# Kernel tuning notes

Measured on AMD Instinct MI355X. Metric: run time of the kernel, lower is better.

## Reference

```python
import jax, jax.numpy as jnp
import numpy as np

TEMPERATURE = 8.0  # sqrt(d_head=64)


def setup_inputs() -> dict:
    key = jax.random.key(0)
    kq, kk, kv, km = jax.random.split(key, 4)
    B, N, L, D = 2, 16, 2048, 64
    q = jax.random.normal(kq, (B, N, L, D), dtype=jnp.float32)
    k = jax.random.normal(kk, (B, N, L, D), dtype=jnp.float32)
    v = jax.random.normal(kv, (B, N, L, D), dtype=jnp.float32)
    mask = jax.random.randint(km, (B, N, L, L), 0, 2).astype(jnp.bool_)
    return {"q": q, "k": k, "v": v, "mask": mask}


def reference(q, k, v, mask):
    # attn = (q @ k^T) / temperature, shape [b, n, lq, lk]
    attn = jnp.einsum("bnqd,bnkd->bnqk", q, k) / TEMPERATURE
    attn = jnp.where(mask, -jnp.inf, attn)
    attn = jax.nn.softmax(attn, axis=-1)
    attn = jnp.where(mask, 0.0, attn)
    # dropout is identity in eval/reference mode
    output = jnp.einsum("bnqk,bnkd->bnqd", attn, v)
    return (output, attn)
```

## Files before the change

kernel.cpp:

```cpp
#include <hip/hip_runtime.h>
#include <math.h>

#define L 2048
#define D 64
#define MT 32
#define KT 128
#define NT 256
#define QSTRIDE 72
#define KSTRIDE 72
#define VSTRIDE 136
#define PSTRIDE 136

typedef short bf16x8 __attribute__((ext_vector_type(8)));
typedef float f32x4  __attribute__((ext_vector_type(4)));

__device__ inline short f2bf(float f) {
    union { float f; unsigned u; } x; x.f = f;
    unsigned r = x.u + 0x7fffu + ((x.u >> 16) & 1u);
    return (short)(r >> 16);
}

__global__ __launch_bounds__(NT) void sdpa_mfma(
    const float* __restrict__ q,
    const float* __restrict__ k,
    const float* __restrict__ v,
    const int*   __restrict__ mask,
    float* __restrict__ out,
    float* __restrict__ attn)
{
    const int bid  = blockIdx.x;
    const int bn   = bid >> 6;
    const int qt   = bid & 63;
    const int row0 = qt * MT;
    const int tid  = threadIdx.x;
    const int wave = tid >> 6;
    const int lane = tid & 63;
    const int lq   = lane & 15;
    const int lg   = lane >> 4;

    __shared__ short Qs[MT * QSTRIDE];
    __shared__ short KV[KT * KSTRIDE];
    __shared__ short Ps[MT * PSTRIDE];
    __shared__ float sums_w[4][MT];
    __shared__ float inv_s[MT];

    const float* qg = q + ((size_t)bn * L + row0) * D;
    const float* kg = k + (size_t)bn * L * D;
    const float* vg = v + (size_t)bn * L * D;
    const int*   mg = mask + ((size_t)bn * L + row0) * L;
    float*       ag = attn + ((size_t)bn * L + row0) * L;

    {
        const int r = tid >> 3, c8 = (tid & 7) * 8;
        const float4* src = (const float4*)(qg + r * D + c8);
        float4 a = src[0], b = src[1];
        bf16x8 t;
        t[0]=f2bf(a.x); t[1]=f2bf(a.y); t[2]=f2bf(a.z); t[3]=f2bf(a.w);
        t[4]=f2bf(b.x); t[5]=f2bf(b.y); t[6]=f2bf(b.z); t[7]=f2bf(b.w);
        *(bf16x8*)&Qs[r * QSTRIDE + c8] = t;
    }
    __syncthreads();

    bf16x8 qa[2][2];
    #pragma unroll
    for (int r = 0; r < 2; ++r)
        #pragma unroll
        for (int s = 0; s < 2; ++s)
            qa[r][s] = *(bf16x8*)&Qs[(r*16 + lq) * QSTRIDE + s*32 + lg*8];

    float sumreg[2][4] = {};
    for (int kt = 0; kt < L / KT; ++kt) {
        const int kb = kt * KT;
        __syncthreads();
        {
            const int r = tid >> 3, c8 = (tid & 7) * 8;
            #pragma unroll
            for (int it = 0; it < 4; ++it) {
                const int rr = r + it * 32;
                const float4* src = (const float4*)(kg + (size_t)(kb + rr) * D + c8);
                float4 a = src[0], b = src[1];
                bf16x8 t;
                t[0]=f2bf(a.x); t[1]=f2bf(a.y); t[2]=f2bf(a.z); t[3]=f2bf(a.w);
                t[4]=f2bf(b.x); t[5]=f2bf(b.y); t[6]=f2bf(b.z); t[7]=f2bf(b.w);
                *(bf16x8*)&KV[rr * KSTRIDE + c8] = t;
            }
        }
        __syncthreads();
        f32x4 acc[2][2] = {};
        #pragma unroll
        for (int s = 0; s < 2; ++s) {
            bf16x8 b0 = *(bf16x8*)&KV[((wave*2+0)*16 + lq) * KSTRIDE + s*32 + lg*8];
            bf16x8 b1 = *(bf16x8*)&KV[((wave*2+1)*16 + lq) * KSTRIDE + s*32 + lg*8];
            acc[0][0] = __builtin_amdgcn_mfma_f32_16x16x32_bf16(qa[0][s], b0, acc[0][0], 0, 0, 0);
            acc[0][1] = __builtin_amdgcn_mfma_f32_16x16x32_bf16(qa[0][s], b1, acc[0][1], 0, 0, 0);
            acc[1][0] = __builtin_amdgcn_mfma_f32_16x16x32_bf16(qa[1][s], b0, acc[1][0], 0, 0, 0);
            acc[1][1] = __builtin_amdgcn_mfma_f32_16x16x32_bf16(qa[1][s], b1, acc[1][1], 0, 0, 0);
        }
        #pragma unroll
        for (int r = 0; r < 2; ++r)
            #pragma unroll
            for (int cc = 0; cc < 2; ++cc) {
                const int col = kb + (wave*2+cc)*16 + lq;
                #pragma unroll
                for (int i = 0; i < 4; ++i) {
                    const int rowl = r*16 + lg*4 + i;
                    const int m = mg[(size_t)rowl * L + col];
                    const float e = m ? 0.f : __expf(acc[r][cc][i] * 0.125f);
                    sumreg[r][i] += e;
                }
            }
    }
    #pragma unroll
    for (int off = 1; off < 16; off <<= 1)
        #pragma unroll
        for (int r = 0; r < 2; ++r)
            #pragma unroll
            for (int i = 0; i < 4; ++i)
                sumreg[r][i] += __shfl_xor(sumreg[r][i], off, 64);
    if (lq == 0)
        #pragma unroll
        for (int r = 0; r < 2; ++r)
            #pragma unroll
            for (int i = 0; i < 4; ++i)
                sums_w[wave][r*16 + lg*4 + i] = sumreg[r][i];
    __syncthreads();
    if (tid < MT) {
        const float s = sums_w[0][tid] + sums_w[1][tid] + sums_w[2][tid] + sums_w[3][tid];
        inv_s[tid] = 1.0f / s;
    }
    __syncthreads();

    f32x4 of[2] = {};
    for (int kt = 0; kt < L / KT; ++kt) {
        const int kb = kt * KT;
        __syncthreads();
        {
            const int r = tid >> 3, c8 = (tid & 7) * 8;
            #pragma unroll
            for (int it = 0; it < 4; ++it) {
                const int rr = r + it * 32;
                const float4* src = (const float4*)(kg + (size_t)(kb + rr) * D + c8);
                float4 a = src[0], b = src[1];
                bf16x8 t;
                t[0]=f2bf(a.x); t[1]=f2bf(a.y); t[2]=f2bf(a.z); t[3]=f2bf(a.w);
                t[4]=f2bf(b.x); t[5]=f2bf(b.y); t[6]=f2bf(b.z); t[7]=f2bf(b.w);
                *(bf16x8*)&KV[rr * KSTRIDE + c8] = t;
            }
        }
        __syncthreads();
        f32x4 acc[2][2] = {};
        #pragma unroll
        for (int s = 0; s < 2; ++s) {
            bf16x8 b0 = *(bf16x8*)&KV[((wave*2+0)*16 + lq) * KSTRIDE + s*32 + lg*8];
            bf16x8 b1 = *(bf16x8*)&KV[((wave*2+1)*16 + lq) * KSTRIDE + s*32 + lg*8];
            acc[0][0] = __builtin_amdgcn_mfma_f32_16x16x32_bf16(qa[0][s], b0, acc[0][0], 0, 0, 0);
            acc[0][1] = __builtin_amdgcn_mfma_f32_16x16x32_bf16(qa[0][s], b1, acc[0][1], 0, 0, 0);
            acc[1][0] = __builtin_amdgcn_mfma_f32_16x16x32_bf16(qa[1][s], b0, acc[1][0], 0, 0, 0);
            acc[1][1] = __builtin_amdgcn_mfma_f32_16x16x32_bf16(qa[1][s], b1, acc[1][1], 0, 0, 0);
        }
        __syncthreads();
        {
            const int d = tid & 63;
            #pragma unroll
            for (int it = 0; it < 4; ++it) {
                const int kgi = (tid >> 6) + it * 4;
                bf16x8 t;
                #pragma unroll
                for (int j = 0; j < 8; ++j)
                    t[j] = f2bf(vg[(size_t)(kb + kgi*8 + j) * D + d]);
                *(bf16x8*)&KV[d * VSTRIDE + kgi * 8] = t;
            }
        }
        #pragma unroll
        for (int r = 0; r < 2; ++r)
            #pragma unroll
            for (int cc = 0; cc < 2; ++cc) {
                const int colL = (wave*2+cc)*16 + lq;
                const int col  = kb + colL;
                #pragma unroll
                for (int i = 0; i < 4; ++i) {
                    const int rowl = r*16 + lg*4 + i;
                    const int m = mg[(size_t)rowl * L + col];
                    const float e = m ? 0.f : __expf(acc[r][cc][i] * 0.125f);
                    const float p = e * inv_s[rowl];
                    ag[(size_t)rowl * L + col] = p;
                    Ps[rowl * PSTRIDE + colL] = f2bf(p);
                }
            }
        __syncthreads();
        #pragma unroll
        for (int s2 = 0; s2 < 4; ++s2) {
            bf16x8 vb  = *(bf16x8*)&KV[(wave*16 + lq) * VSTRIDE + s2*32 + lg*8];
            bf16x8 pa0 = *(bf16x8*)&Ps[(lq)      * PSTRIDE + s2*32 + lg*8];
            bf16x8 pa1 = *(bf16x8*)&Ps[(16 + lq) * PSTRIDE + s2*32 + lg*8];
            of[0] = __builtin_amdgcn_mfma_f32_16x16x32_bf16(pa0, vb, of[0], 0, 0, 0);
            of[1] = __builtin_amdgcn_mfma_f32_16x16x32_bf16(pa1, vb, of[1], 0, 0, 0);
        }
    }
    #pragma unroll
    for (int r = 0; r < 2; ++r)
        #pragma unroll
        for (int i = 0; i < 4; ++i) {
            const int rowl = r*16 + lg*4 + i;
            out[((size_t)bn * L + row0 + rowl) * D + wave*16 + lq] = of[r][i];
        }
}

extern "C" void kernel_launch(void* const* d_in, const int* in_sizes, int n_in,
                              void* d_out, int out_size, void* d_ws, size_t ws_size,
                              hipStream_t stream) {
    const float* q    = (const float*)d_in[0];
    const float* k    = (const float*)d_in[1];
    const float* v    = (const float*)d_in[2];
    const int*   mask = (const int*)d_in[3];

    float* out = (float*)d_out;
    const int rows = in_sizes[0] / D;
    float* attn = out + (size_t)rows * D;

    const int nblocks = rows / MT;
    sdpa_mfma<<<nblocks, NT, 0, stream>>>(q, k, v, mask, out, attn);
}
```

Baseline: 1.428 ms.

## Pre-convert Q/K/V to swizzled bf16 and fuse softmax into one pass

Adds pre-kernels that convert Q and K to bf16 with an XOR-swizzled layout and transpose V into per-tile bf16 blocks. The main kernel then does a single pass over K tiles, writing unnormalized exponentials to attn and accumulating P·V, and normalizes the output at the end. A separate kernel rescales the whole attn matrix by the per-row inverse sum. This removes the second QK^T pass, the repeated fp32-to-bf16 conversion and the strided V gather, and it vectorizes the mask reads and attn writes. In exchange the large attn matrix is read and written a second time, and there are extra launches and workspace traffic.

```diff
diff --git a/kernel.cpp b/kernel.cpp
--- a/kernel.cpp
+++ b/kernel.cpp
@@ -6,27 +6,73 @@
 #define MT 32
 #define KT 128
 #define NT 256
-#define QSTRIDE 72
-#define KSTRIDE 72
-#define VSTRIDE 136
-#define PSTRIDE 136
 
 typedef short bf16x8 __attribute__((ext_vector_type(8)));
+typedef short bf16x4 __attribute__((ext_vector_type(4)));
 typedef float f32x4  __attribute__((ext_vector_type(4)));
 
-__device__ inline short f2bf(float f) {
+#define MFMA16 __builtin_amdgcn_mfma_f32_16x16x32_bf16
+
+__device__ __forceinline__ short f2bf(float f) {
     union { float f; unsigned u; } x; x.f = f;
     unsigned r = x.u + 0x7fffu + ((x.u >> 16) & 1u);
     return (short)(r >> 16);
 }
 
-__global__ __launch_bounds__(NT) void sdpa_mfma(
-    const float* __restrict__ q,
-    const float* __restrict__ k,
-    const float* __restrict__ v,
+__global__ __launch_bounds__(NT) void conv_swz(
+    const float* __restrict__ src, short* __restrict__ dst, int nrows)
+{
+    int g = blockIdx.x * NT + threadIdx.x;
+    if (g >= nrows * 8) return;
+    int row = g >> 3, c = g & 7;
+    const float4* s4 = (const float4*)(src + (size_t)row * D + c * 8);
+    float4 a = s4[0], b = s4[1];
+    bf16x8 t;
+    t[0]=f2bf(a.x); t[1]=f2bf(a.y); t[2]=f2bf(a.z); t[3]=f2bf(a.w);
+    t[4]=f2bf(b.x); t[5]=f2bf(b.y); t[6]=f2bf(b.z); t[7]=f2bf(b.w);
+    *(bf16x8*)(dst + (size_t)row * D + ((c ^ (row & 7)) * 8)) = t;
+}
+
+__global__ __launch_bounds__(NT) void vtrans(
+    const float* __restrict__ v, short* __restrict__ vt)
+{
+    const int h  = blockIdx.x >> 4;
+    const int kt = blockIdx.x & 15;
+    const float* src = v + ((size_t)h * L + (size_t)kt * KT) * D;
+    short* dst = vt + (size_t)blockIdx.x * (D * KT);
+    __shared__ short Vs[KT * 68];
+    const int t = threadIdx.x;
+    {
+        const int r = t & 127, seg = t >> 7;
+        const float4* s4 = (const float4*)(src + r * D + seg * 32);
+        #pragma unroll
+        for (int kq = 0; kq < 8; ++kq) {
+            float4 a = s4[kq];
+            bf16x4 b;
+            b[0]=f2bf(a.x); b[1]=f2bf(a.y); b[2]=f2bf(a.z); b[3]=f2bf(a.w);
+            *(bf16x4*)(Vs + r * 68 + seg * 32 + kq * 4) = b;
+        }
+    }
+    __syncthreads();
+    #pragma unroll
+    for (int j = 0; j < 4; ++j) {
+        const int cg = t + NT * j;
+        const int d = cg >> 4, c = cg & 15;
+        bf16x8 o;
+        #pragma unroll
+        for (int jj = 0; jj < 8; ++jj) o[jj] = Vs[(c * 8 + jj) * 68 + d];
+        *(bf16x8*)(dst + d * KT + ((c ^ (d & 7)) * 8)) = o;
+    }
+}
+
+__global__ __launch_bounds__(NT, 4) void sdpa_fused(
+    const short* __restrict__ qb,
+    const short* __restrict__ kb,
+    const short* __restrict__ vtb,
     const int*   __restrict__ mask,
     float* __restrict__ out,
-    float* __restrict__ attn)
+    float* __restrict__ attn,
+    float* __restrict__ invs)
 {
     const int bid  = blockIdx.x;
     const int bn   = bid >> 6;
@@ -37,173 +83,145 @@
     const int lane = tid & 63;
     const int lq   = lane & 15;
     const int lg   = lane >> 4;
-
-    __shared__ short Qs[MT * QSTRIDE];
-    __shared__ short KV[KT * KSTRIDE];
-    __shared__ short Ps[MT * PSTRIDE];
-    __shared__ float sums_w[4][MT];
-    __shared__ float inv_s[MT];
-
-    const float* qg = q + ((size_t)bn * L + row0) * D;
-    const float* kg = k + (size_t)bn * L * D;
-    const float* vg = v + (size_t)bn * L * D;
+    const int swz  = lq & 7;
+
+    __shared__ __align__(16) char smem[40960];
+    short* Kb = (short*)smem;
+    short* Vb = (short*)(smem + 16384);
+    short* Ps = (short*)(smem + 32768);
+    short* Qt = Ps;
+    float* sums_w = (float*)(smem + 32768);
+    float* inv_l  = (float*)(smem + 32768 + 512);
+
+    const short* qh = qb  + (size_t)bn * L * D;
+    const short* kh = kb  + (size_t)bn * L * D;
     const int*   mg = mask + ((size_t)bn * L + row0) * L;
     float*       ag = attn + ((size_t)bn * L + row0) * L;
 
-    {
-        const int r = tid >> 3, c8 = (tid & 7) * 8;
-        const float4* src = (const float4*)(qg + r * D + c8);
-        float4 a = src[0], b = src[1];
-        bf16x8 t;
-        t[0]=f2bf(a.x); t[1]=f2bf(a.y); t[2]=f2bf(a.z); t[3]=f2bf(a.w);
-        t[4]=f2bf(b.x); t[5]=f2bf(b.y); t[6]=f2bf(b.z); t[7]=f2bf(b.w);
-        *(bf16x8*)&Qs[r * QSTRIDE + c8] = t;
-    }
-    __syncthreads();
-
-    bf16x8 qa[2][2];
-    #pragma unroll
-    for (int r = 0; r < 2; ++r)
+    *(bf16x8*)(Qt + tid * 8) = *(const bf16x8*)(qh + (size_t)row0 * D + tid * 8);
+    __syncthreads();
+    bf16x8 qf[2][2];
+    #pragma unroll
+    for (int qq = 0; qq < 2; ++qq)
         #pragma unroll
         for (int s = 0; s < 2; ++s)
-            qa[r][s] = *(bf16x8*)&Qs[(r*16 + lq) * QSTRIDE + s*32 + lg*8];
-
-    float sumreg[2][4] = {};
+            qf[qq][s] = *(const bf16x8*)(Qt + (qq*16 + lq) * D + (((s*4 + lg) ^ swz) * 8));
+    __syncthreads();
+
+    f32x4 of[2] = {};
+    float sumreg[2] = {0.f, 0.f};
+
     for (int kt = 0; kt < L / KT; ++kt) {
-        const int kb = kt * KT;
+        const int kb0 = kt * KT;
+        const short* ks = kh + (size_t)kb0 * D;
+        const short* vs = vtb + ((size_t)bn * (L / KT) + kt) * (D * KT);
+        bf16x8 kr[4], vr[4];
+        #pragma unroll
+        for (int c = 0; c < 4; ++c) {
+            kr[c] = *(const bf16x8*)(ks + (c * NT + tid) * 8);
+            vr[c] = *(const bf16x8*)(vs + (c * NT + tid) * 8);
+        }
+        int4 m4[2][2];
+        #pragma unroll
+        for (int kk = 0; kk < 2; ++kk)
+            #pragma unroll
+            for (int qq = 0; qq < 2; ++qq)
+                m4[kk][qq] = *(const int4*)(mg + (size_t)(qq*16 + lq) * L
+                                               + kb0 + wave*32 + kk*16 + lg*4);
         __syncthreads();
-        {
-            const int r = tid >> 3, c8 = (tid & 7) * 8;
+        #pragma unroll
+        for (int c = 0; c < 4; ++c) {
+            *(bf16x8*)(Kb + (c * NT + tid) * 8) = kr[c];
+            *(bf16x8*)(Vb + (c * NT + tid) * 8) = vr[c];
+        }
+        __syncthreads();
+
+        f32x4 acc[2][2] = {};
+        __builtin_amdgcn_s_setprio(1);
+        #pragma unroll
+        for (int s = 0; s < 2; ++s) {
+            bf16x8 a0 = *(const bf16x8*)(Kb + (wave*32 + lq)      * D + (((s*4 + lg) ^ swz) * 8));
+            bf16x8 a1 = *(const bf16x8*)(Kb + (wave*32 + 16 + lq) * D + (((s*4 + lg) ^ swz) * 8));
+            acc[0][0] = MFMA16(a0, qf[0][s], acc[0][0], 0, 0, 0);
+            acc[0][1] = MFMA16(a0, qf[1][s], acc[0][1], 0, 0, 0);
+            acc[1][0] = MFMA16(a1, qf[0][s], acc[1][0], 0, 0, 0);
+            acc[1][1] = MFMA16(a1, qf[1][s], acc[1][1], 0, 0, 0);
+        }
+        __builtin_amdgcn_s_setprio(0);
+
+        #pragma unroll
+        for (int kk = 0; kk < 2; ++kk)
             #pragma unroll
-            for (int it = 0; it < 4; ++it) {
-                const int rr = r + it * 32;
-                const float4* src = (const float4*)(kg + (size_t)(kb + rr) * D + c8);
-                float4 a = src[0], b = src[1];
-                bf16x8 t;
-                t[0]=f2bf(a.x); t[1]=f2bf(a.y); t[2]=f2bf(a.z); t[3]=f2bf(a.w);
-                t[4]=f2bf(b.x); t[5]=f2bf(b.y); t[6]=f2bf(b.z); t[7]=f2bf(b.w);
-                *(bf16x8*)&KV[rr * KSTRIDE + c8] = t;
-            }
-        }
-        __syncthreads();
-        f32x4 acc[2][2] = {};
-        #pragma unroll
-        for (int s = 0; s < 2; ++s) {
-            bf16x8 b0 = *(bf16x8*)&KV[((wave*2+0)*16 + lq) * KSTRIDE + s*32 + lg*8];
-            bf16x8 b1 = *(bf16x8*)&KV[((wave*2+1)*16 + lq) * KSTRIDE + s*32 + lg*8];
-            acc[0][0] = __builtin_amdgcn_mfma_f32_16x16x32_bf16(qa[0][s], b0, acc[0][0], 0, 0, 0);
-            acc[0][1] = __builtin_amdgcn_mfma_f32_16x16x32_bf16(qa[0][s], b1, acc[0][1], 0, 0, 0);
-            acc[1][0] = __builtin_amdgcn_mfma_f32_16x16x32_bf16(qa[1][s], b0, acc[1][0], 0, 0, 0);
-            acc[1][1] = __builtin_amdgcn_mfma_f32_16x16x32_bf16(qa[1][s], b1, acc[1][1], 0, 0, 0);
-        }
-        #pragma unroll
-        for (int r = 0; r < 2; ++r)
-            #pragma unroll
-            for (int cc = 0; cc < 2; ++cc) {
-                const int col = kb + (wave*2+cc)*16 + lq;
-                #pragma unroll
-                for (int i = 0; i < 4; ++i) {
-                    const int rowl = r*16 + lg*4 + i;
-                    const int m = mg[(size_t)rowl * L + col];
-                    const float e = m ? 0.f : __expf(acc[r][cc][i] * 0.125f);
-                    sumreg[r][i] += e;
-                }
-            }
-    }
-    #pragma unroll
-    for (int off = 1; off < 16; off <<= 1)
-        #pragma unroll
-        for (int r = 0; r < 2; ++r)
-            #pragma unroll
-            for (int i = 0; i < 4; ++i)
-                sumreg[r][i] += __shfl_xor(sumreg[r][i], off, 64);
-    if (lq == 0)
-        #pragma unroll
-        for (int r = 0; r < 2; ++r)
-            #pragma unroll
-            for (int i = 0; i < 4; ++i)
-                sums_w[wave][r*16 + lg*4 + i] = sumreg[r][i];
-    __syncthreads();
-    if (tid < MT) {
-        const float s = sums_w[0][tid] + sums_w[1][tid] + sums_w[2][tid] + sums_w[3][tid];
-        inv_s[tid] = 1.0f / s;
-    }
-    __syncthreads();
-
-    f32x4 of[2] = {};
-    for (int kt = 0; kt < L / KT; ++kt) {
-        const int kb = kt * KT;
-        __syncthreads();
-        {
-            const int r = tid >> 3, c8 = (tid & 7) * 8;
-            #pragma unroll
-            for (int it = 0; it < 4; ++it) {
-                const int rr = r + it * 32;
-                const float4* src = (const float4*)(kg + (size_t)(kb + rr) * D + c8);
-                float4 a = src[0], b = src[1];
-                bf16x8 t;
-                t[0]=f2bf(a.x); t[1]=f2bf(a.y); t[2]=f2bf(a.z); t[3]=f2bf(a.w);
-                t[4]=f2bf(b.x); t[5]=f2bf(b.y); t[6]=f2bf(b.z); t[7]=f2bf(b.w);
-                *(bf16x8*)&KV[rr * KSTRIDE + c8] = t;
-            }
-        }
-        __syncthreads();
-        f32x4 acc[2][2] = {};
-        #pragma unroll
-        for (int s = 0; s < 2; ++s) {
-            bf16x8 b0 = *(bf16x8*)&KV[((wave*2+0)*16 + lq) * KSTRIDE + s*32 + lg*8];
-            bf16x8 b1 = *(bf16x8*)&KV[((wave*2+1)*16 + lq) * KSTRIDE + s*32 + lg*8];
-            acc[0][0] = __builtin_amdgcn_mfma_f32_16x16x32_bf16(qa[0][s], b0, acc[0][0], 0, 0, 0);
-            acc[0][1] = __builtin_amdgcn_mfma_f32_16x16x32_bf16(qa[0][s], b1, acc[0][1], 0, 0, 0);
-            acc[1][0] = __builtin_amdgcn_mfma_f32_16x16x32_bf16(qa[1][s], b0, acc[1][0], 0, 0, 0);
-            acc[1][1] = __builtin_amdgcn_mfma_f32_16x16x32_bf16(qa[1][s], b1, acc[1][1], 0, 0, 0);
-        }
-        __syncthreads();
-        {
-            const int d = tid & 63;
-            #pragma unroll
-            for (int it = 0; it < 4; ++it) {
-                const int kgi = (tid >> 6) + it * 4;
-                bf16x8 t;
-                #pragma unroll
-                for (int j = 0; j < 8; ++j)
-                    t[j] = f2bf(vg[(size_t)(kb + kgi*8 + j) * D + d]);
-                *(bf16x8*)&KV[d * VSTRIDE + kgi * 8] = t;
-            }
-        }
-        #pragma unroll
-        for (int r = 0; r < 2; ++r)
-            #pragma unroll
-            for (int cc = 0; cc < 2; ++cc) {
-                const int colL = (wave*2+cc)*16 + lq;
-                const int col  = kb + colL;
-                #pragma unroll
-                for (int i = 0; i < 4; ++i) {
-                    const int rowl = r*16 + lg*4 + i;
-                    const int m = mg[(size_t)rowl * L + col];
-                    const float e = m ? 0.f : __expf(acc[r][cc][i] * 0.125f);
-                    const float p = e * inv_s[rowl];
-                    ag[(size_t)rowl * L + col] = p;
-                    Ps[rowl * PSTRIDE + colL] = f2bf(p);
-                }
+            for (int qq = 0; qq < 2; ++qq) {
+                const int qrow = qq*16 + lq;
+                const int colL = wave*32 + kk*16 + lg*4;
+                const int4 m = m4[kk][qq];
+                const f32x4 a = acc[kk][qq];
+                const float e0 = m.x ? 0.f : __expf(a[0] * 0.125f);
+                const float e1 = m.y ? 0.f : __expf(a[1] * 0.125f);
+                const float e2 = m.z ? 0.f : __expf(a[2] * 0.125f);
+                const float e3 = m.w ? 0.f : __expf(a[3] * 0.125f);
+                sumreg[qq] += (e0 + e1) + (e2 + e3);
+                float4 ev; ev.x = e0; ev.y = e1; ev.z = e2; ev.w = e3;
+                *(float4*)(ag + (size_t)qrow * L + kb0 + colL) = ev;
+                bf16x4 pb;
+                pb[0]=f2bf(e0); pb[1]=f2bf(e1); pb[2]=f2bf(e2); pb[3]=f2bf(e3);
+                *(bf16x4*)(Ps + qrow * KT + (colL ^ (swz * 8))) = pb;
             }
         __syncthreads();
+
+        __builtin_amdgcn_s_setprio(1);
         #pragma unroll
         for (int s2 = 0; s2 < 4; ++s2) {
-            bf16x8 vb  = *(bf16x8*)&KV[(wave*16 + lq) * VSTRIDE + s2*32 + lg*8];
-            bf16x8 pa0 = *(bf16x8*)&Ps[(lq)      * PSTRIDE + s2*32 + lg*8];
-            bf16x8 pa1 = *(bf16x8*)&Ps[(16 + lq) * PSTRIDE + s2*32 + lg*8];
-            of[0] = __builtin_amdgcn_mfma_f32_16x16x32_bf16(pa0, vb, of[0], 0, 0, 0);
-            of[1] = __builtin_amdgcn_mfma_f32_16x16x32_bf16(pa1, vb, of[1], 0, 0, 0);
-        }
-    }
+            const int ch = ((s2*4 + lg) ^ swz) * 8;
+            bf16x8 vb = *(const bf16x8*)(Vb + (wave*16 + lq) * KT + ch);
+            bf16x8 p0 = *(const bf16x8*)(Ps + lq * KT + ch);
+            bf16x8 p1 = *(const bf16x8*)(Ps + (16 + lq) * KT + ch);
+            of[0] = MFMA16(p0, vb, of[0], 0, 0, 0);
+            of[1] = MFMA16(p1, vb, of[1], 0, 0, 0);
+        }
+        __builtin_amdgcn_s_setprio(0);
+    }
+
+    #pragma unroll
+    for (int qq = 0; qq < 2; ++qq) {
+        sumreg[qq] += __shfl_xor(sumreg[qq], 16, 64);
+        sumreg[qq] += __shfl_xor(sumreg[qq], 32, 64);
+    }
+    __syncthreads();
+    if (lane < 16) {
+        sums_w[wave * 32 + lq]      = sumreg[0];
+        sums_w[wave * 32 + 16 + lq] = sumreg[1];
+    }
+    __syncthreads();
+    if (tid < MT) {
+        const float s = sums_w[tid] + sums_w[32 + tid] + sums_w[64 + tid] + sums_w[96 + tid];
+        const float inv = 1.0f / s;
+        inv_l[tid] = inv;
+        invs[(size_t)bn * L + row0 + tid] = inv;
+    }
+    __syncthreads();
     #pragma unroll
     for (int r = 0; r < 2; ++r)
         #pragma unroll
         for (int i = 0; i < 4; ++i) {
-            const int rowl = r*16 + lg*4 + i;
-            out[((size_t)bn * L + row0 + rowl) * D + wave*16 + lq] = of[r][i];
-        }
+            const int qrow = r*16 + lg*4 + i;
+            out[((size_t)bn * L + row0 + qrow) * D + wave*16 + lq] = of[r][i] * inv_l[qrow];
+        }
+}
+
+__global__ __launch_bounds__(NT) void scale_attn(
+    float* __restrict__ attn, const float* __restrict__ invs, long long total4)
+{
+    long long i = (long long)blockIdx.x * NT + threadIdx.x;
+    const long long stride = (long long)gridDim.x * NT;
+    float4* a4 = (float4*)attn;
+    for (; i < total4; i += stride) {
+        const float inv = invs[i >> 9];
+        float4 t = a4[i];
+        t.x *= inv; t.y *= inv; t.z *= inv; t.w *= inv;
+        a4[i] = t;
+    }
 }
 
 extern "C" void kernel_launch(void* const* d_in, const int* in_sizes, int n_in,
@@ -218,6 +236,15 @@
     const int rows = in_sizes[0] / D;
     float* attn = out + (size_t)rows * D;
 
-    const int nblocks = rows / MT;
-    sdpa_mfma<<<nblocks, NT, 0, stream>>>(q, k, v, mask, out, attn);
-}
+    short* qb   = (short*)d_ws;
+    short* kb   = qb  + (size_t)rows * D;
+    short* vtb  = kb  + (size_t)rows * D;
+    float* invs = (float*)(vtb + (size_t)rows * D);
+
+    const int heads = rows / L;
+    conv_swz<<<rows * 8 / NT, NT, 0, stream>>>(q, qb, rows);
+    conv_swz<<<rows * 8 / NT, NT, 0, stream>>>(k, kb, rows);
+    vtrans<<<heads * (L / KT), NT, 0, stream>>>(v, vtb);
+    sdpa_fused<<<rows / MT, NT, 0, stream>>>(qb, kb, vtb, mask, out, attn, invs);
+    scale_attn<<<8192, NT, 0, stream>>>(attn, invs, (long long)rows * (L / 4));
+}
```

After: 1.193 ms. -16.4%, faster.
